# Optimization experiments

Measured on AMD Instinct MI355X. Metric: run time of the kernel, lower is better.

The kernel has to match this reference:

```python
import jax, jax.numpy as jnp
import numpy as np

B, H, W, C = 2, 128, 128, 128
K = 3            # window_size
NB = K * K       # neighbor_count = 9
RP = 8           # relative_position_dim
HID = 128        # edge hidden = max(256//2, 128)
EIN = 3 * C + RP # edge_input_dim = 392
CLIP = 3.0
GEPS = 1e-06     # gate_eps
LNE = 1e-05      # LayerNorm eps


def _ln(x, g, b):
    m = x.mean(-1, keepdims=True)
    v = ((x - m) ** 2).mean(-1, keepdims=True)
    return (x - m) * jax.lax.rsqrt(v + LNE) * g + b


def setup_inputs() -> dict:
    key = jax.random.key(0)
    ks = jax.random.split(key, 12)
    f32 = jnp.float32
    inp = {
        'tokens': jax.random.normal(ks[0], (B, H, W, C), dtype=f32),
        'ln1_g': jnp.ones((C,), f32), 'ln1_b': jnp.zeros((C,), f32),
        'ln2_g': jnp.ones((C,), f32), 'ln2_b': jnp.zeros((C,), f32),
        'rel_pos': 0.02 * jax.random.normal(ks[1], (NB, RP), dtype=f32),
        'dW1': 0.01 * jax.random.normal(ks[2], (EIN, HID), dtype=f32),
        'db1': jnp.zeros((HID,), f32),
        'dW2': 0.01 * jax.random.normal(ks[3], (HID, 1), dtype=f32),
        'db2': jnp.zeros((1,), f32),
        'rW1': 0.01 * jax.random.normal(ks[4], (EIN, HID), dtype=f32),
        'rb1': jnp.zeros((HID,), f32),
        'rW2': 0.01 * jax.random.normal(ks[5], (HID, 1), dtype=f32),
        'rb2': jnp.zeros((1,), f32),
        'vW': 0.01 * jax.random.normal(ks[6], (C, C), dtype=f32),
        'vb': jnp.zeros((C,), f32),
        'oW': 0.01 * jax.random.normal(ks[7], (C, C), dtype=f32),
        'ob': jnp.zeros((C,), f32),
        'eml_gamma': jnp.asarray(0.1, f32),
        'eml_lam': jnp.asarray(1.0, f32),
        'eml_bias': jnp.asarray(-0.3, f32),
    }
    return inp


def _edge_mlp(x, W1, b1, W2, b2):
    h = jax.nn.gelu(jnp.einsum('blnd,dh->blnh', x, W1) + b1, approximate=False)
    return jnp.einsum('blnh,ho->blno', h, W2) + b2


def _forward(tokens, ln1_g, ln1_b, ln2_g, ln2_b, rel_pos, dW1, db1, dW2, db2,
             rW1, rb1, rW2, rb2, vW, vb, oW, ob, eml_gamma, eml_lam, eml_bias,
             warmup_eta=1.0):
    Bh, Hh, Wh, Ch = tokens.shape
    L = Hh * Wh
    normalized = _ln(tokens, ln1_g, ln1_b)
    flat = normalized.reshape(Bh, L, Ch)
    # Unfold(kernel=3, padding=1): gather 9 shifted views, then replicate torch's
    # reshape of the (C, 9)-ordered channel axis into (9, C).
    pad = jnp.pad(normalized, ((0, 0), (1, 1), (1, 1), (0, 0)))
    shifts = [pad[:, i:i + Hh, j:j + Wh, :] for i in range(K) for j in range(K)]
    nbhd = jnp.stack(shifts, axis=-1)                       # [B,H,W,C,9]
    nbhd = nbhd.reshape(Bh, L, Ch * NB).reshape(Bh, L, NB, Ch)  # torch reshape semantics
    center = jnp.broadcast_to(flat[:, :, None, :], nbhd.shape)
    rel = jnp.broadcast_to(rel_pos[None, None], (Bh, L, NB, rel_pos.shape[-1]))
    edge_features = jnp.concatenate([center, nbhd, center - nbhd, rel], axis=-1)
    drive = _edge_mlp(edge_features, dW1, db1, dW2, db2)[..., 0]        # [B,L,9]
    resistance = _edge_mlp(edge_features, rW1, rb1, rW2, rb2)[..., 0]   # [B,L,9]
    # EML unit (Ohm's-law style gate): clamp(eta*gamma*drive/(lambda*softplus(R)+eps)+bias)
    energy = jnp.clip(
        warmup_eta * (eml_gamma * drive) / (eml_lam * jax.nn.softplus(resistance) + GEPS)
        + eml_bias, -CLIP, CLIP)
    gate = jax.nn.sigmoid(energy)                                        # [B,L,9]
    values = jnp.einsum('blnc,cd->blnd', nbhd, vW) + vb                  # [B,L,9,C]
    gate_mass = jnp.maximum(gate.sum(axis=2), GEPS)                      # [B,L]
    message = jnp.einsum('bln,blnc->blc', gate, values) / gate_mass[..., None]
    update = (jnp.einsum('blc,cd->bld', message, oW) + ob).reshape(Bh, Hh, Wh, Ch)
    output = _ln(tokens + update, ln2_g, ln2_b)  # dropout is identity at eval
    return output


def reference(tokens, ln1_g, ln1_b, ln2_g, ln2_b, rel_pos, dW1, db1, dW2, db2,
              rW1, rb1, rW2, rb2, vW, vb, oW, ob, eml_gamma, eml_lam, eml_bias):
    return _forward(tokens, ln1_g, ln1_b, ln2_g, ln2_b, rel_pos, dW1, db1, dW2, db2,
                    rW1, rb1, rW2, rb2, vW, vb, oW, ob, eml_gamma, eml_lam, eml_bias)
```

## Files before the change

kernel.cpp:

```cpp
#include <hip/hip_runtime.h>


#define USHORT unsigned short
#define AW 152

typedef __attribute__((ext_vector_type(8)))  __bf16 v8bf;
typedef __attribute__((ext_vector_type(8)))  USHORT v8u;
typedef __attribute__((ext_vector_type(16))) float  v16f;

__device__ __forceinline__ USHORT f2bf(float f) {
    unsigned v; __builtin_memcpy(&v, &f, 4);
    v += 0x7FFFu + ((v >> 16) & 1u);
    return (USHORT)(v >> 16);
}

template <int C>
__device__ __forceinline__ float dpps(float x) {
    return __int_as_float(
        __builtin_amdgcn_update_dpp(0, __float_as_int(x), C, 0xf, 0xf, true));
}
__device__ __forceinline__ float red32half(float x) {
    x += dpps<0x111>(x);
    x += dpps<0x112>(x);
    x += dpps<0x114>(x);
    x += dpps<0x118>(x);
    x += dpps<0x142>(x);
    return x;
}
__device__ __forceinline__ float red64(float x) {
    x = red32half(x);
    x += dpps<0x143>(x);
    return x;
}
__device__ __forceinline__ float bcast63(float x) {
    return __int_as_float(__builtin_amdgcn_readlane(__float_as_int(x), 63));
}

__global__ __launch_bounds__(256) void k_setup(
    const float* __restrict__ tok, const float* __restrict__ ln1g,
    const float* __restrict__ ln1b,
    const float* __restrict__ dW1, const float* __restrict__ db1,
    const float* __restrict__ rW1, const float* __restrict__ rb1,
    const float* __restrict__ rel, const float* __restrict__ dW2,
    const float* __restrict__ rW2, const float* __restrict__ vW,
    const float* __restrict__ vb,  const float* __restrict__ oW,
    USHORT* __restrict__ norm,
    USHORT* __restrict__ WnTg, USHORT* __restrict__ WcTg, USHORT* __restrict__ VTg,
    float* __restrict__ preg, float* __restrict__ vboWg, float* __restrict__ w2g)
{
    const int blk = blockIdx.x, t = threadIdx.x;
    if (blk >= 354) {
        const int p = (blk - 354) * 4 + (t >> 6);
        const int lane = t & 63;
        const float2 x = ((const float2*)(tok + (size_t)p * 128))[lane];
        float s = x.x + x.y;
        for (int m = 1; m < 64; m <<= 1) s += __shfl_xor(s, m);
        const float mean = s * (1.f / 128.f);
        const float d0 = x.x - mean, d1 = x.y - mean;
        float q = d0 * d0 + d1 * d1;
        for (int m = 1; m < 64; m <<= 1) q += __shfl_xor(q, m);
        const float rstd = rsqrtf(q * (1.f / 128.f) + 1e-5f);
        const float2 gg = ((const float2*)ln1g)[lane], bb = ((const float2*)ln1b)[lane];
        ((unsigned*)norm)[(size_t)p * 64 + lane] =
            (unsigned)f2bf(d0 * rstd * gg.x + bb.x) |
            ((unsigned)f2bf(d1 * rstd * gg.y + bb.y) << 16);
        return;
    }
    if (blk < 72) {
        int idx = blk * 256 + t;
        int n = ((idx >> 4) * 7282) >> 16;
        int k = idx - n * 144;
        int r = k >> 4, tt = k & 15, c2 = r + 9 * tt;
        float acc = 0.f;
        if (c2 < 128)
            for (int j = 0; j < 128; ++j) acc += vW[c2 * 128 + j] * oW[j * 128 + n];
        VTg[idx] = f2bf(acc);
    } else if (blk < 216) {
        int idx = (blk - 72) * 256 + t;
        int n = ((idx >> 4) * 7282) >> 16;
        int k = idx - n * 144;
        int r = k >> 4, tt = k & 15, c2 = r + 9 * tt;
        int col = n & 127;
        const float* W = (n < 128) ? dW1 : rW1;
        float val = 0.f;
        if (c2 < 128) val = W[(128 + c2) * 128 + col] - W[(256 + c2) * 128 + col];
        WnTg[idx] = f2bf(val);
    } else if (blk < 344) {
        int idx = (blk - 216) * 256 + t;
        int n = idx >> 7, c = idx & 127, col = n & 127;
        const float* W = (n < 128) ? dW1 : rW1;
        WcTg[idx] = f2bf(W[c * 128 + col] + W[(256 + c) * 128 + col]);
    } else if (blk < 353) {
        int n2 = blk - 344; int h = t;
        float acc;
        if (h < 128) {
            acc = db1[h];
            for (int r = 0; r < 8; ++r) acc += rel[n2 * 8 + r] * dW1[(384 + r) * 128 + h];
        } else {
            int hh = h - 128;
            acc = rb1[hh];
            for (int r = 0; r < 8; ++r) acc += rel[n2 * 8 + r] * rW1[(384 + r) * 128 + hh];
        }
        preg[n2 * 256 + h] = acc;
    } else {
        if (t < 128) {
            float acc = 0.f;
            for (int j = 0; j < 128; ++j) acc += vb[j] * oW[j * 128 + t];
            vboWg[t] = acc;
            w2g[t] = dW2[t];
            w2g[128 + t] = rW2[t];
        }
    }
}

__device__ __forceinline__ void gather_load(
    uint2 (&pf)[9], const USHORT* __restrict__ nb,
    int n2, int y, int bI, int tid)
{
    const int x = tid >> 2, q = tid & 3;
    #pragma unroll
    for (int r = 0; r < 9; ++r) {
        int u = 2 * n2 + r;
        int n = (u >= 18) ? (u - 18) : ((u >= 9) ? (u - 9) : u);
        int v = n2 * 128 + r;
        int c0 = (v * 7282) >> 16;
        int dyq = (n * 22) >> 6;
        int dx = n - 3 * dyq - 1;
        int dy = dyq - 1;
        int sy = y + dy, sx = x + dx;
        bool ok = ((unsigned)sy < 128u) && ((unsigned)sx < 128u);
        int e0 = (c0 & ~1) + 4 * q;
        size_t gidx = ((size_t)((bI * 128 + (ok ? sy : 0)) * 128 + (ok ? sx : 0))) * 128 + e0;
        const unsigned* gp = (const unsigned*)nb + (gidx >> 1);
        unsigned dw0 = gp[0], dw1 = gp[1];
        pf[r].x = ok ? dw0 : 0u;
        pf[r].y = ok ? dw1 : 0u;
    }
}

__device__ __forceinline__ void gather_store(
    USHORT* __restrict__ Ash, const uint2 (&pf)[9], int n2, int tid)
{
    const int x = tid >> 2, q = tid & 3;
    #pragma unroll
    for (int r = 0; r < 9; ++r) {
        int v = n2 * 128 + r;
        int c0 = (v * 7282) >> 16;
        unsigned dw0 = pf[r].x, dw1 = pf[r].y;
        unsigned nxt = (unsigned)__shfl_down((int)dw0, 1);
        unsigned o0, o1;
        if (c0 & 1) { o0 = (dw0 >> 16) | (dw1 << 16); o1 = (dw1 >> 16) | (nxt << 16); }
        else        { o0 = dw0;                       o1 = dw1; }
        *(uint2*)(Ash + x * AW + 16 * r + 4 * q) = make_uint2(o0, o1);
    }
}

__global__ __launch_bounds__(512, 2) void k_edge(
    const float* __restrict__ tok, const float* __restrict__ ln2g,
    const float* __restrict__ ln2b, const USHORT* __restrict__ nb,
    const USHORT* __restrict__ WnTg, const USHORT* __restrict__ WcTg,
    const USHORT* __restrict__ VTg, const float* __restrict__ preg,
    const float* __restrict__ vboWg, const float* __restrict__ w2g,
    const float* __restrict__ db2p, const float* __restrict__ rb2p,
    const float* __restrict__ gmp, const float* __restrict__ lmp,
    const float* __restrict__ bip, const float* __restrict__ obp,
    float* __restrict__ out)
{
    extern __shared__ char smem[];
    USHORT* Wsh  = (USHORT*)smem;
    USHORT* Ash  = (USHORT*)(smem + 77824);
    USHORT* VTl  = (USHORT*)(smem + 116736);
    float*  w2L  = (float*)(smem + 155648);
    float*  dP   = (float*)(smem + 156672);
    float*  rP   = (float*)(smem + 157696);
    float*  gateL= (float*)(smem + 158720);
    float*  sgL  = (float*)(smem + 159232);
    float*  updF = (float*)smem;

    const int tid = threadIdx.x;
    const int lane = tid & 63, wave = tid >> 6, hi = lane >> 5, l31 = lane & 31;
    const int mw = wave & 1, nw = wave >> 1;
    const int blk = blockIdx.x;
    const int bI = blk >> 7;
    const int y = ((blk & 7) << 4) | ((blk >> 3) & 15);
    const int p0 = (bI * 128 + y) * 128;

    for (int i = tid; i < 4096; i += 512) {
        int n = i >> 4, kv = i & 15;
        *(v8u*)(Wsh + n * AW + kv * 8) = *(const v8u*)(WcTg + n * 128 + kv * 8);
    }
    for (int i = tid; i < 2048; i += 512) {
        int x = i >> 4, kv = i & 15;
        *(v8u*)(Ash + x * AW + kv * 8) = *(const v8u*)(nb + (size_t)(p0 + x) * 128 + kv * 8);
    }
    for (int i = tid; i < 2304; i += 512) {
        int n = (i * 3641) >> 16;
        int kv = i - n * 18;
        *(v8u*)(VTl + n * AW + kv * 8) = *(const v8u*)(VTg + n * 144 + kv * 8);
    }
    if (tid < 256) w2L[tid] = w2g[tid];
    if (tid < 128) sgL[tid] = 0.f;
    __syncthreads();

    v16f cp[2][2];
    #pragma unroll
    for (int a = 0; a < 2; ++a)
        for (int b = 0; b < 2; ++b)
            for (int e = 0; e < 16; ++e) cp[a][b][e] = 0.f;
    #pragma unroll
    for (int ks = 0; ks < 8; ++ks) {
        v8bf af0 = *(const v8bf*)(Ash + (mw * 64 + l31) * AW + ks * 16 + hi * 8);
        v8bf af1 = *(const v8bf*)(Ash + (mw * 64 + 32 + l31) * AW + ks * 16 + hi * 8);
        v8bf bf0 = *(const v8bf*)(Wsh + (nw * 64 + l31) * AW + ks * 16 + hi * 8);
        v8bf bf1 = *(const v8bf*)(Wsh + (nw * 64 + 32 + l31) * AW + ks * 16 + hi * 8);
        cp[0][0] = __builtin_amdgcn_mfma_f32_32x32x16_bf16(af0, bf0, cp[0][0], 0, 0, 0);
        cp[0][1] = __builtin_amdgcn_mfma_f32_32x32x16_bf16(af0, bf1, cp[0][1], 0, 0, 0);
        cp[1][0] = __builtin_amdgcn_mfma_f32_32x32x16_bf16(af1, bf0, cp[1][0], 0, 0, 0);
        cp[1][1] = __builtin_amdgcn_mfma_f32_32x32x16_bf16(af1, bf1, cp[1][1], 0, 0, 0);
    }
    __syncthreads();

    for (int i = tid; i < 4608; i += 512) {
        int n = (i * 3641) >> 16;
        int kv = i - n * 18;
        *(v8u*)(Wsh + n * AW + kv * 8) = *(const v8u*)(WnTg + n * 144 + kv * 8);
    }
    {
        uint2 pf0[9];
        gather_load(pf0, nb, 0, y, bI, tid);
        gather_store(Ash, pf0, 0, tid);
    }

    const float gmv = gmp[0], lmv = lmp[0], biv = bip[0];
    const float db2v = db2p[0], rb2v = rb2p[0];
    const float wv0 = w2L[nw * 64 + l31];
    const float wv1 = w2L[nw * 64 + 32 + l31];

    v16f acc3[2];
    #pragma unroll
    for (int a = 0; a < 2; ++a)
        for (int e = 0; e < 16; ++e) acc3[a][e] = 0.f;

    float* sumBase = ((nw < 2) ? dP : rP) + (nw & 1) * 128;

    __syncthreads();

    for (int n2 = 0; n2 < 9; ++n2) {
        const float pv0 = preg[n2 * 256 + nw * 64 + l31];
        const float pv1 = preg[n2 * 256 + nw * 64 + 32 + l31];

        uint2 pf[9];
        if (n2 < 8) gather_load(pf, nb, n2 + 1, y, bI, tid);

        v16f acc[2][2];
        #pragma unroll
        for (int a = 0; a < 2; ++a)
            for (int b = 0; b < 2; ++b) acc[a][b] = cp[a][b];
        v16f P[2];
        #pragma unroll
        for (int a = 0; a < 2; ++a)
            for (int e = 0; e < 16; ++e) P[a][e] = 0.f;
        #pragma unroll
        for (int ks = 0; ks < 9; ++ks) {
            v8bf af0 = *(const v8bf*)(Ash + (mw * 64 + l31) * AW + ks * 16 + hi * 8);
            v8bf af1 = *(const v8bf*)(Ash + (mw * 64 + 32 + l31) * AW + ks * 16 + hi * 8);
            v8bf bf0 = *(const v8bf*)(Wsh + (nw * 64 + l31) * AW + ks * 16 + hi * 8);
            v8bf bf1 = *(const v8bf*)(Wsh + (nw * 64 + 32 + l31) * AW + ks * 16 + hi * 8);
            v8bf vf  = *(const v8bf*)(VTl + (nw * 32 + l31) * AW + ks * 16 + hi * 8);
            acc[0][0] = __builtin_amdgcn_mfma_f32_32x32x16_bf16(af0, bf0, acc[0][0], 0, 0, 0);
            acc[0][1] = __builtin_amdgcn_mfma_f32_32x32x16_bf16(af0, bf1, acc[0][1], 0, 0, 0);
            acc[1][0] = __builtin_amdgcn_mfma_f32_32x32x16_bf16(af1, bf0, acc[1][0], 0, 0, 0);
            acc[1][1] = __builtin_amdgcn_mfma_f32_32x32x16_bf16(af1, bf1, acc[1][1], 0, 0, 0);
            P[0] = __builtin_amdgcn_mfma_f32_32x32x16_bf16(af0, vf, P[0], 0, 0, 0);
            P[1] = __builtin_amdgcn_mfma_f32_32x32x16_bf16(af1, vf, P[1], 0, 0, 0);
        }
        #pragma unroll
        for (int mt = 0; mt < 2; ++mt) {
            float part[16];
            #pragma unroll
            for (int rr = 0; rr < 16; ++rr) {
                float h0 = acc[mt][0][rr] + pv0;
                float h1 = acc[mt][1][rr] + pv1;
                float s0 = __builtin_amdgcn_rcpf(1.f + __expf(-1.702f * h0));
                float s1 = __builtin_amdgcn_rcpf(1.f + __expf(-1.702f * h1));
                part[rr] = h0 * s0 * wv0 + h1 * s1 * wv1;
            }
            #pragma unroll
            for (int rr = 0; rr < 16; ++rr) part[rr] = red32half(part[rr]);
            if (l31 == 31) {
                float* t0 = sumBase + ((mw * 2 + mt) * 2 + hi) * 16;
                *(float4*)(t0 +  0) = make_float4(part[0],  part[1],  part[2],  part[3]);
                *(float4*)(t0 +  4) = make_float4(part[4],  part[5],  part[6],  part[7]);
                *(float4*)(t0 +  8) = make_float4(part[8],  part[9],  part[10], part[11]);
                *(float4*)(t0 + 12) = make_float4(part[12], part[13], part[14], part[15]);
            }
        }
        __syncthreads();
        if (n2 < 8) gather_store(Ash, pf, n2 + 1, tid);
        if (tid < 128) {
            int w32 = tid & 31;
            int slot = (((tid >> 6) * 2 + ((tid >> 5) & 1)) * 2 + ((w32 >> 2) & 1)) * 16
                       + ((w32 & 3) | (((w32 >> 3) & 3) << 2));
            float d = dP[slot] + dP[128 + slot] + db2v;
            float rr = rP[slot] + rP[128 + slot] + rb2v;
            float sp = fmaxf(rr, 0.f) + log1pf(__expf(-fabsf(rr)));
            float e = gmv * d / (lmv * sp + 1e-6f) + biv;
            e = fminf(fmaxf(e, -3.f), 3.f);
            float gt = 1.f / (1.f + __expf(-e));
            gateL[tid] = gt; sgL[tid] += gt;
        }
        __syncthreads();
        #pragma unroll
        for (int mt = 0; mt < 2; ++mt) {
            const float4* gq = (const float4*)&gateL[mw * 64 + mt * 32 + 4 * hi];
            float4 ga = gq[0], gb = gq[2], gc = gq[4], gd = gq[6];
            float gs[16] = {ga.x, ga.y, ga.z, ga.w, gb.x, gb.y, gb.z, gb.w,
                            gc.x, gc.y, gc.z, gc.w, gd.x, gd.y, gd.z, gd.w};
            #pragma unroll
            for (int rr = 0; rr < 16; ++rr) acc3[mt][rr] += gs[rr] * P[mt][rr];
        }
    }

    __syncthreads();
    if (tid < 128) {
        float s = sgL[tid];
        float m = fmaxf(s, 1e-6f);
        dP[tid] = 1.f / m;
        rP[tid] = s / m;
    }
    __syncthreads();

    {
        const int colc = nw * 32 + l31;
        const float vbw = vboWg[colc], obv = obp[colc];
        #pragma unroll
        for (int mt = 0; mt < 2; ++mt) {
            const int base = mw * 64 + mt * 32 + 4 * hi;
            const float4* iq = (const float4*)&dP[base];
            const float4* sq = (const float4*)&rP[base];
            float4 ia = iq[0], ib = iq[2], ic = iq[4], id = iq[6];
            float4 sa = sq[0], sb = sq[2], sc = sq[4], sd = sq[6];
            float iv[16] = {ia.x, ia.y, ia.z, ia.w, ib.x, ib.y, ib.z, ib.w,
                            ic.x, ic.y, ic.z, ic.w, id.x, id.y, id.z, id.w};
            float sv[16] = {sa.x, sa.y, sa.z, sa.w, sb.x, sb.y, sb.z, sb.w,
                            sc.x, sc.y, sc.z, sc.w, sd.x, sd.y, sd.z, sd.w};
            #pragma unroll
            for (int rr = 0; rr < 16; ++rr) {
                int row = base + (rr & 3) + 8 * (rr >> 2);
                updF[row * 128 + colc] = acc3[mt][rr] * iv[rr] + vbw * sv[rr] + obv;
            }
        }
    }
    __syncthreads();

    const float g20 = ln2g[lane], g21 = ln2g[lane + 64];
    const float b20 = ln2b[lane], b21 = ln2b[lane + 64];
    for (int q2 = 0; q2 < 16; ++q2) {
        int p = wave * 16 + q2;
        size_t gp = (size_t)(p0 + p) * 128;
        float x0 = tok[gp + lane]      + updF[p * 128 + lane];
        float x1 = tok[gp + lane + 64] + updF[p * 128 + lane + 64];
        float mean = bcast63(red64(x0 + x1)) * (1.f / 128.f);
        float d0 = x0 - mean, d1 = x1 - mean;
        float rstd = rsqrtf(bcast63(red64(d0 * d0 + d1 * d1)) * (1.f / 128.f) + 1e-5f);
        out[gp + lane]      = d0 * rstd * g20 + b20;
        out[gp + lane + 64] = d1 * rstd * g21 + b21;
    }
}

extern "C" void kernel_launch(void* const* d_in, const int* in_sizes, int n_in,
                              void* d_out, int out_size, void* d_ws, size_t ws_size,
                              hipStream_t stream) {
    const float* tok  = (const float*)d_in[0];
    const float* ln1g = (const float*)d_in[1];
    const float* ln1b = (const float*)d_in[2];
    const float* ln2g = (const float*)d_in[3];
    const float* ln2b = (const float*)d_in[4];
    const float* rel  = (const float*)d_in[5];
    const float* dW1  = (const float*)d_in[6];
    const float* db1  = (const float*)d_in[7];
    const float* dW2  = (const float*)d_in[8];
    const float* db2  = (const float*)d_in[9];
    const float* rW1  = (const float*)d_in[10];
    const float* rb1  = (const float*)d_in[11];
    const float* rW2  = (const float*)d_in[12];
    const float* rb2  = (const float*)d_in[13];
    const float* vW   = (const float*)d_in[14];
    const float* vb   = (const float*)d_in[15];
    const float* oW   = (const float*)d_in[16];
    const float* ob   = (const float*)d_in[17];
    const float* gm   = (const float*)d_in[18];
    const float* lm   = (const float*)d_in[19];
    const float* bi   = (const float*)d_in[20];
    float* out = (float*)d_out;

    char* w = (char*)d_ws;
    USHORT* norm = (USHORT*)w; w += 8388608;
    USHORT* WnTg = (USHORT*)w; w += 73728;
    USHORT* WcTg = (USHORT*)w; w += 65536;
    USHORT* VTg  = (USHORT*)w; w += 36864;
    float*  preg = (float*)w;  w += 9216;
    float*  vboWg= (float*)w;  w += 512;
    float*  w2g  = (float*)w;  w += 1024;

    hipFuncSetAttribute((const void*)k_edge,
                        hipFuncAttributeMaxDynamicSharedMemorySize, 159744);

    hipLaunchKernelGGL(k_setup, dim3(8546), dim3(256), 0, stream,
                       tok, ln1g, ln1b, dW1, db1, rW1, rb1, rel, dW2, rW2,
                       vW, vb, oW, norm, WnTg, WcTg, VTg, preg, vboWg, w2g);
    hipLaunchKernelGGL(k_edge, dim3(256), dim3(512), 159744, stream,
                       tok, ln2g, ln2b, norm, WnTg, WcTg, VTg, preg, vboWg, w2g,
                       db2, rb2, gm, lm, bi, ob, out);
}
```

Measured before the change: 189.2 us.

## Accumulate gate-weighted neighbor sums before a single value-projection GEMM

Instead of running the value/output projection MFMA for each of the 9 neighbors and then weighting by the gate, each thread now accumulates gate-weighted neighbor features in fp32 registers. A single projection GEMM runs after the loop on the bf16-rounded sum. This relies on linearity to cut the per-neighbor MFMA work. It also double-buffers the gathered neighbor tile (reusing the old VT buffer), so the next neighbor's store no longer overwrites the tile still being read. The cost is 36 extra accumulator registers per thread and an extra bf16 rounding of the aggregated features.

Result: no change. 185.8 us (-1.8%).

```diff
diff --git a/kernel.cpp b/kernel.cpp
--- a/kernel.cpp
+++ b/kernel.cpp
@@ -139,7 +139,7 @@
 }
 
 __device__ __forceinline__ void gather_store(
-    USHORT* __restrict__ Ash, const uint2 (&pf)[9], int n2, int tid)
+    USHORT* __restrict__ Adst, const uint2 (&pf)[9], int n2, int tid)
 {
     const int x = tid >> 2, q = tid & 3;
     #pragma unroll
@@ -151,7 +151,7 @@
         unsigned o0, o1;
         if (c0 & 1) { o0 = (dw0 >> 16) | (dw1 << 16); o1 = (dw1 >> 16) | (nxt << 16); }
         else        { o0 = dw0;                       o1 = dw1; }
-        *(uint2*)(Ash + x * AW + 16 * r + 4 * q) = make_uint2(o0, o1);
+        *(uint2*)(Adst + x * AW + 16 * r + 4 * q) = make_uint2(o0, o1);
     }
 }
 
@@ -168,8 +168,8 @@
 {
     extern __shared__ char smem[];
     USHORT* Wsh  = (USHORT*)smem;
-    USHORT* Ash  = (USHORT*)(smem + 77824);
-    USHORT* VTl  = (USHORT*)(smem + 116736);
+    USHORT* Ash0 = (USHORT*)(smem + 77824);
+    USHORT* Ash1 = (USHORT*)(smem + 116736);
     float*  w2L  = (float*)(smem + 155648);
     float*  dP   = (float*)(smem + 156672);
     float*  rP   = (float*)(smem + 157696);
@@ -191,12 +191,7 @@
     }
     for (int i = tid; i < 2048; i += 512) {
         int x = i >> 4, kv = i & 15;
-        *(v8u*)(Ash + x * AW + kv * 8) = *(const v8u*)(nb + (size_t)(p0 + x) * 128 + kv * 8);
-    }
-    for (int i = tid; i < 2304; i += 512) {
-        int n = (i * 3641) >> 16;
-        int kv = i - n * 18;
-        *(v8u*)(VTl + n * AW + kv * 8) = *(const v8u*)(VTg + n * 144 + kv * 8);
+        *(v8u*)(Ash0 + x * AW + kv * 8) = *(const v8u*)(nb + (size_t)(p0 + x) * 128 + kv * 8);
     }
     if (tid < 256) w2L[tid] = w2g[tid];
     if (tid < 128) sgL[tid] = 0.f;
@@ -209,8 +204,8 @@
             for (int e = 0; e < 16; ++e) cp[a][b][e] = 0.f;
     #pragma unroll
     for (int ks = 0; ks < 8; ++ks) {
-        v8bf af0 = *(const v8bf*)(Ash + (mw * 64 + l31) * AW + ks * 16 + hi * 8);
-        v8bf af1 = *(const v8bf*)(Ash + (mw * 64 + 32 + l31) * AW + ks * 16 + hi * 8);
+        v8bf af0 = *(const v8bf*)(Ash0 + (mw * 64 + l31) * AW + ks * 16 + hi * 8);
+        v8bf af1 = *(const v8bf*)(Ash0 + (mw * 64 + 32 + l31) * AW + ks * 16 + hi * 8);
         v8bf bf0 = *(const v8bf*)(Wsh + (nw * 64 + l31) * AW + ks * 16 + hi * 8);
         v8bf bf1 = *(const v8bf*)(Wsh + (nw * 64 + 32 + l31) * AW + ks * 16 + hi * 8);
         cp[0][0] = __builtin_amdgcn_mfma_f32_32x32x16_bf16(af0, bf0, cp[0][0], 0, 0, 0);
@@ -228,7 +223,7 @@
     {
         uint2 pf0[9];
         gather_load(pf0, nb, 0, y, bI, tid);
-        gather_store(Ash, pf0, 0, tid);
+        gather_store(Ash0, pf0, 0, tid);
     }
 
     const float gmv = gmp[0], lmv = lmp[0], biv = bip[0];
@@ -236,16 +231,18 @@
     const float wv0 = w2L[nw * 64 + l31];
     const float wv1 = w2L[nw * 64 + 32 + l31];
 
-    v16f acc3[2];
-    #pragma unroll
-    for (int a = 0; a < 2; ++a)
-        for (int e = 0; e < 16; ++e) acc3[a][e] = 0.f;
+    float G[36];
+    #pragma unroll
+    for (int j = 0; j < 36; ++j) G[j] = 0.f;
+    const int grow = tid >> 2, gq = tid & 3;
 
     float* sumBase = ((nw < 2) ? dP : rP) + (nw & 1) * 128;
 
     __syncthreads();
 
     for (int n2 = 0; n2 < 9; ++n2) {
+        USHORT* Acur = (n2 & 1) ? Ash1 : Ash0;
+        USHORT* Anxt = (n2 & 1) ? Ash0 : Ash1;
         const float pv0 = preg[n2 * 256 + nw * 64 + l31];
         const float pv1 = preg[n2 * 256 + nw * 64 + 32 + l31];
 
@@ -256,23 +253,16 @@
         #pragma unroll
         for (int a = 0; a < 2; ++a)
             for (int b = 0; b < 2; ++b) acc[a][b] = cp[a][b];
-        v16f P[2];
-        #pragma unroll
-        for (int a = 0; a < 2; ++a)
-            for (int e = 0; e < 16; ++e) P[a][e] = 0.f;
         #pragma unroll
         for (int ks = 0; ks < 9; ++ks) {
-            v8bf af0 = *(const v8bf*)(Ash + (mw * 64 + l31) * AW + ks * 16 + hi * 8);
-            v8bf af1 = *(const v8bf*)(Ash + (mw * 64 + 32 + l31) * AW + ks * 16 + hi * 8);
+            v8bf af0 = *(const v8bf*)(Acur + (mw * 64 + l31) * AW + ks * 16 + hi * 8);
+            v8bf af1 = *(const v8bf*)(Acur + (mw * 64 + 32 + l31) * AW + ks * 16 + hi * 8);
             v8bf bf0 = *(const v8bf*)(Wsh + (nw * 64 + l31) * AW + ks * 16 + hi * 8);
             v8bf bf1 = *(const v8bf*)(Wsh + (nw * 64 + 32 + l31) * AW + ks * 16 + hi * 8);
-            v8bf vf  = *(const v8bf*)(VTl + (nw * 32 + l31) * AW + ks * 16 + hi * 8);
             acc[0][0] = __builtin_amdgcn_mfma_f32_32x32x16_bf16(af0, bf0, acc[0][0], 0, 0, 0);
             acc[0][1] = __builtin_amdgcn_mfma_f32_32x32x16_bf16(af0, bf1, acc[0][1], 0, 0, 0);
             acc[1][0] = __builtin_amdgcn_mfma_f32_32x32x16_bf16(af1, bf0, acc[1][0], 0, 0, 0);
             acc[1][1] = __builtin_amdgcn_mfma_f32_32x32x16_bf16(af1, bf1, acc[1][1], 0, 0, 0);
-            P[0] = __builtin_amdgcn_mfma_f32_32x32x16_bf16(af0, vf, P[0], 0, 0, 0);
-            P[1] = __builtin_amdgcn_mfma_f32_32x32x16_bf16(af1, vf, P[1], 0, 0, 0);
         }
         #pragma unroll
         for (int mt = 0; mt < 2; ++mt) {
@@ -296,7 +286,7 @@
             }
         }
         __syncthreads();
-        if (n2 < 8) gather_store(Ash, pf, n2 + 1, tid);
+        if (n2 < 8) gather_store(Anxt, pf, n2 + 1, tid);
         if (tid < 128) {
             int w32 = tid & 31;
             int slot = (((tid >> 6) * 2 + ((tid >> 5) & 1)) * 2 + ((w32 >> 2) & 1)) * 16
@@ -310,18 +300,40 @@
             gateL[tid] = gt; sgL[tid] += gt;
         }
         __syncthreads();
+        {
+            const float g = gateL[grow];
+            const USHORT* Ar = Acur + grow * AW + gq * 36;
+            #pragma unroll
+            for (int j = 0; j < 9; ++j) {
+                uint2 wv = *(const uint2*)(Ar + 4 * j);
+                float v0 = __int_as_float((int)(wv.x << 16));
+                float v1 = __int_as_float((int)(wv.x & 0xFFFF0000u));
+                float v2 = __int_as_float((int)(wv.y << 16));
+                float v3 = __int_as_float((int)(wv.y & 0xFFFF0000u));
+                G[4 * j + 0] += g * v0;
+                G[4 * j + 1] += g * v1;
+                G[4 * j + 2] += g * v2;
+                G[4 * j + 3] += g * v3;
+            }
+        }
+    }
+
+    __syncthreads();
+
+    {
+        USHORT* dst = Ash0 + grow * AW + gq * 36;
         #pragma unroll
-        for (int mt = 0; mt < 2; ++mt) {
-            const float4* gq = (const float4*)&gateL[mw * 64 + mt * 32 + 4 * hi];
-            float4 ga = gq[0], gb = gq[2], gc = gq[4], gd = gq[6];
-            float gs[16] = {ga.x, ga.y, ga.z, ga.w, gb.x, gb.y, gb.z, gb.w,
-                            gc.x, gc.y, gc.z, gc.w, gd.x, gd.y, gd.z, gd.w};
-            #pragma unroll
-            for (int rr = 0; rr < 16; ++rr) acc3[mt][rr] += gs[rr] * P[mt][rr];
-        }
-    }
-
-    __syncthreads();
+        for (int j = 0; j < 9; ++j) {
+            unsigned lo = (unsigned)f2bf(G[4 * j + 0]) | ((unsigned)f2bf(G[4 * j + 1]) << 16);
+            unsigned hi2 = (unsigned)f2bf(G[4 * j + 2]) | ((unsigned)f2bf(G[4 * j + 3]) << 16);
+            *(uint2*)(dst + 4 * j) = make_uint2(lo, hi2);
+        }
+    }
+    for (int i = tid; i < 2304; i += 512) {
+        int n = (i * 3641) >> 16;
+        int kv = i - n * 18;
+        *(v8u*)(Ash1 + n * AW + kv * 8) = *(const v8u*)(VTg + n * 144 + kv * 8);
+    }
     if (tid < 128) {
         float s = sgL[tid];
         float m = fmaxf(s, 1e-6f);
@@ -329,6 +341,19 @@
         rP[tid] = s / m;
     }
     __syncthreads();
+
+    v16f P[2];
+    #pragma unroll
+    for (int a = 0; a < 2; ++a)
+        for (int e = 0; e < 16; ++e) P[a][e] = 0.f;
+    #pragma unroll
+    for (int ks = 0; ks < 9; ++ks) {
+        v8bf af0 = *(const v8bf*)(Ash0 + (mw * 64 + l31) * AW + ks * 16 + hi * 8);
+        v8bf af1 = *(const v8bf*)(Ash0 + (mw * 64 + 32 + l31) * AW + ks * 16 + hi * 8);
+        v8bf vf  = *(const v8bf*)(Ash1 + (nw * 32 + l31) * AW + ks * 16 + hi * 8);
+        P[0] = __builtin_amdgcn_mfma_f32_32x32x16_bf16(af0, vf, P[0], 0, 0, 0);
+        P[1] = __builtin_amdgcn_mfma_f32_32x32x16_bf16(af1, vf, P[1], 0, 0, 0);
+    }
 
     {
         const int colc = nw * 32 + l31;
@@ -347,7 +372,7 @@
             #pragma unroll
             for (int rr = 0; rr < 16; ++rr) {
                 int row = base + (rr & 3) + 8 * (rr >> 2);
-                updF[row * 128 + colc] = acc3[mt][rr] * iv[rr] + vbw * sv[rr] + obv;
+                updF[row * 128 + colc] = P[mt][rr] * iv[rr] + vbw * sv[rr] + obv;
             }
         }
     }
```
